# Performance work log

Hardware: AMD Instinct MI355X
Metric: run time of the kernel (lower is better)

The kernel has to match this reference:

```python
import jax, jax.numpy as jnp
import numpy as np

HEADS = 4
DIM_HEAD = 32


def setup_inputs() -> dict:
    key = jax.random.key(0)
    k1, k2, k3, k4 = jax.random.split(key, 4)
    dim = 256
    hidden = HEADS * DIM_HEAD  # 128
    x = jax.random.normal(k1, (4, dim, 64, 64), dtype=jnp.float32)
    # 1x1 convs are channel-mixing matmuls; store weights as [out_ch, in_ch]
    w_qkv = jax.random.normal(k2, (3 * hidden, dim), dtype=jnp.float32) * (dim ** -0.5)
    w_out = jax.random.normal(k3, (dim, hidden), dtype=jnp.float32) * (hidden ** -0.5)
    b_out = jax.random.normal(k4, (dim,), dtype=jnp.float32) * 0.02
    return {"x": x, "w_qkv": w_qkv, "w_out": w_out, "b_out": b_out}


def reference(x, w_qkv, w_out, b_out):
    b, c, h, w = x.shape
    n = h * w
    scale = DIM_HEAD ** -0.5
    xf = x.reshape(b, c, n)                                   # b c n
    qkv = jnp.einsum('oc,bcn->bon', w_qkv, xf)                # b (3*H*D) n
    q, k, v = jnp.split(qkv, 3, axis=1)                       # each b (H*D) n
    q = q.reshape(b, HEADS, DIM_HEAD, n) * scale              # b h d n
    k = k.reshape(b, HEADS, DIM_HEAD, n)
    v = v.reshape(b, HEADS, DIM_HEAD, n)
    sim = jnp.einsum('bhdi,bhdj->bhij', q, k)                 # b h n n
    attn = jax.nn.softmax(sim, axis=-1)                       # stable max-subtract inside
    out = jnp.einsum('bhij,bhdj->bhdi', attn, v)              # b h d n
    out = out.reshape(b, HEADS * DIM_HEAD, n)                 # b (h d) n
    out = jnp.einsum('oc,bcn->bon', w_out, out) + b_out[None, :, None]
    return out.reshape(b, -1, h, w)
```

## Files before the change

kernel.cpp:

```cpp
#include <hip/hip_runtime.h>
#include <hip/hip_bf16.h>
#include <stdint.h>

#define B_SZ 4
#define C_IN 256
#define N_SP 4096
#define HEADS 4
#define DH 32
#define HID 128

#define BI 128
#define BJ 64
#define JHALF 2048
#define PP 68

typedef short short4v __attribute__((ext_vector_type(4)));
typedef short short8 __attribute__((ext_vector_type(8)));
typedef float f32x4 __attribute__((ext_vector_type(4)));

#if __has_builtin(__builtin_amdgcn_exp2f)
#define EXP2 __builtin_amdgcn_exp2f
#else
#define EXP2 exp2f
#endif

__device__ __forceinline__ short f2bfs(float f) {
  return (short)((__float_as_uint(f) + 0x8000u) >> 16);
}
__device__ __forceinline__ float bfs2f(short s) {
  return __uint_as_float(((uint32_t)(unsigned short)s) << 16);
}
__device__ __forceinline__ short8 ld_frag(const short* p) {
  short4v a = *(const short4v*)p;
  short4v b = *(const short4v*)(p + 4);
  return __builtin_shufflevector(a, b, 0, 1, 2, 3, 4, 5, 6, 7);
}
__device__ __forceinline__ f32x4 mfma16(short8 a, short8 b, f32x4 c) {
  return __builtin_amdgcn_mfma_f32_16x16x32_bf16(a, b, c, 0, 0, 0);
}

__global__ __launch_bounds__(256) void prep_k(
    const float* __restrict__ x, const float* __restrict__ w_qkv,
    const float* __restrict__ w_out,
    short* __restrict__ xh, short* __restrict__ xl,
    short* __restrict__ wqh, short* __restrict__ wql,
    short* __restrict__ woh, short* __restrict__ wol) {
  const int t = threadIdx.x;
  const int bx = blockIdx.x;
  if (bx < 1024) {
    __shared__ float T[64 * 65];
    const int b = bx >> 8, n0 = ((bx >> 2) & 63) * 64, c0 = (bx & 3) * 64;
    const float* xb = x + (size_t)b * C_IN * N_SP;
    {
      const int n = t & 63, cw = t >> 6;
#pragma unroll
      for (int i = 0; i < 16; ++i) {
        const int c = cw * 16 + i;
        T[n * 65 + c] = xb[(size_t)(c0 + c) * N_SP + n0 + n];
      }
    }
    __syncthreads();
    {
      const int n = t >> 2, cg = t & 3;
#pragma unroll
      for (int j = 0; j < 2; ++j) {
        const int c = cg * 16 + j * 8;
        short8 hv, lv;
#pragma unroll
        for (int e = 0; e < 8; ++e) {
          const float v = T[n * 65 + c + e];
          const short hh = f2bfs(v);
          hv[e] = hh;
          lv[e] = f2bfs(v - bfs2f(hh));
        }
        const size_t off = ((size_t)(b * N_SP + n0 + n)) * C_IN + c0 + c;
        *(short8*)(xh + off) = hv;
        *(short8*)(xl + off) = lv;
      }
    }
  } else {
    const int f0 = (bx - 1024) * 8192;
#pragma unroll
    for (int j = 0; j < 32; ++j) {
      const int f = f0 + j * 256 + t;
      float v;
      short *dh, *dl;
      int idx;
      if (f < 384 * 256) { v = w_qkv[f]; dh = wqh; dl = wql; idx = f; }
      else { idx = f - 384 * 256; v = w_out[idx]; dh = woh; dl = wol; }
      const short hh = f2bfs(v);
      dh[idx] = hh;
      dl[idx] = f2bfs(v - bfs2f(hh));
    }
  }
}

__global__ __launch_bounds__(256) void qkv_mfma_k(
    const short* __restrict__ xh, const short* __restrict__ xl,
    const short* __restrict__ wqh, const short* __restrict__ wql,
    short* __restrict__ qt, short* __restrict__ kt, short* __restrict__ vt) {
  const int t = threadIdx.x;
  const int lane = t & 63, w = t >> 6;
  const int l15 = lane & 15, quad = lane >> 4;
  const int osec = blockIdx.y, b = blockIdx.z;
  const int n0 = blockIdx.x * 64 + w * 16;
  const size_t xrow = ((size_t)(b * N_SP + n0 + l15)) * C_IN;
  const size_t wrow = ((size_t)(osec * 128 + l15)) * C_IN;
  const bool isv = (osec == 2);
  const f32x4 zz = {0.f, 0.f, 0.f, 0.f};
  f32x4 acc[8];
#pragma unroll
  for (int ot = 0; ot < 8; ++ot) acc[ot] = zz;

  for (int k0 = 0; k0 < C_IN; k0 += 32) {
    const int ko = k0 + quad * 8;
    const short8 xhf = *(const short8*)(xh + xrow + ko);
    const short8 xlf = *(const short8*)(xl + xrow + ko);
#pragma unroll
    for (int ot = 0; ot < 8; ++ot) {
      const size_t wo = wrow + (size_t)ot * 16 * C_IN + ko;
      const short8 whf = *(const short8*)(wqh + wo);
      const short8 wlf = *(const short8*)(wql + wo);
      if (isv) {
        acc[ot] = mfma16(xhf, whf, acc[ot]);
        acc[ot] = mfma16(xlf, whf, acc[ot]);
        acc[ot] = mfma16(xhf, wlf, acc[ot]);
      } else {
        acc[ot] = mfma16(whf, xhf, acc[ot]);
        acc[ot] = mfma16(whf, xlf, acc[ot]);
        acc[ot] = mfma16(wlf, xhf, acc[ot]);
      }
    }
  }

  if (!isv) {
    const float sc = osec ? 1.f : (0.17677669529663687f * 1.4426950408889634f);
    short* dst = osec ? kt : qt;
    const int n = n0 + l15;
#pragma unroll
    for (int ot = 0; ot < 8; ++ot) {
      const int ol = ot * 16 + quad * 4;
      const int h = ol >> 5, d0 = ol & 31;
      short4v p;
#pragma unroll
      for (int r = 0; r < 4; ++r) p[r] = f2bfs(acc[ot][r] * sc);
      *(short4v*)(dst + ((size_t)(b * HEADS + h) * N_SP + n) * DH + d0) = p;
    }
  } else {
    const int n = n0 + quad * 4;
#pragma unroll
    for (int ot = 0; ot < 8; ++ot) {
      const int ol = ot * 16 + l15;
      const int h = ol >> 5, d = ol & 31;
      short4v p;
#pragma unroll
      for (int r = 0; r < 4; ++r) p[r] = f2bfs(acc[ot][r]);
      *(short4v*)(vt + ((size_t)(b * HEADS + h) * DH + d) * N_SP + n) = p;
    }
  }
}

__global__ __launch_bounds__(256, 2) void attn_k(
    const short* __restrict__ qt, const short* __restrict__ kt,
    const short* __restrict__ vt, float* __restrict__ po,
    float* __restrict__ lws) {
  __shared__ short Ps[BI * PP];
  const int t = threadIdx.x;
  const int lane = t & 63, w = t >> 6;
  const int l15 = lane & 15, quad = lane >> 4;
  const int i0 = blockIdx.x * BI;
  const int bh = blockIdx.y;
  const int part = blockIdx.z;
  const int jbase = part * JHALF;
  const short* qg = qt + ((size_t)bh * N_SP + i0) * DH;
  const short* kg = kt + ((size_t)bh * N_SP + jbase) * DH;
  const short* vg = vt + (size_t)bh * DH * N_SP + jbase;

  short8 bq[2];
#pragma unroll
  for (int tt = 0; tt < 2; ++tt)
    bq[tt] = *(const short8*)(qg + (size_t)(w * 32 + tt * 16 + l15) * DH + quad * 8);

  const f32x4 zz = {0.f, 0.f, 0.f, 0.f};
  f32x4 o_acc[2][2] = {{zz, zz}, {zz, zz}};
  f32x4 l_acc[2] = {zz, zz};
  short8 ones;
#pragma unroll
  for (int e = 0; e < 8; ++e) ones[e] = (short)0x3F80;
  short* prow[2];
#pragma unroll
  for (int tt = 0; tt < 2; ++tt) prow[tt] = Ps + (w * 32 + tt * 16 + l15) * PP;

  short8 akA[4], akB[4], vbA[2][2], vbB[2][2];
#pragma unroll
  for (int jt = 0; jt < 4; ++jt)
    akA[jt] = *(const short8*)(kg + (size_t)(jt * 16 + l15) * DH + quad * 8);
#pragma unroll
  for (int dt = 0; dt < 2; ++dt)
#pragma unroll
    for (int kk = 0; kk < 2; ++kk)
      vbA[dt][kk] = *(const short8*)(vg + (size_t)(dt * 16 + l15) * N_SP + kk * 32 + quad * 8);

  auto body = [&](const short8 (&akc)[4], const short8 (&vbc)[2][2],
                  short8 (&akn)[4], short8 (&vbn)[2][2], int jn) {
    f32x4 sf[2][4];
#pragma unroll
    for (int tt = 0; tt < 2; ++tt)
#pragma unroll
      for (int jt = 0; jt < 4; ++jt) sf[tt][jt] = mfma16(akc[jt], bq[tt], zz);
#pragma unroll
    for (int jt = 0; jt < 4; ++jt)
      akn[jt] = *(const short8*)(kg + (size_t)(jn + jt * 16 + l15) * DH + quad * 8);
#pragma unroll
    for (int dt = 0; dt < 2; ++dt)
#pragma unroll
      for (int kk = 0; kk < 2; ++kk)
        vbn[dt][kk] = *(const short8*)(vg + (size_t)(dt * 16 + l15) * N_SP + jn + kk * 32 + quad * 8);
#pragma unroll
    for (int tt = 0; tt < 2; ++tt)
#pragma unroll
      for (int jt = 0; jt < 4; ++jt) {
        const float e0 = EXP2(sf[tt][jt][0]);
        const float e1 = EXP2(sf[tt][jt][1]);
        const float e2 = EXP2(sf[tt][jt][2]);
        const float e3 = EXP2(sf[tt][jt][3]);
        uint2 pk;
        asm("v_cvt_pk_bf16_f32 %0, %1, %2" : "=v"(pk.x) : "v"(e0), "v"(e1));
        asm("v_cvt_pk_bf16_f32 %0, %1, %2" : "=v"(pk.y) : "v"(e2), "v"(e3));
        *(uint2*)(prow[tt] + jt * 16 + quad * 4) = pk;
      }
    asm volatile("s_waitcnt lgkmcnt(0)" ::: "memory");
    short8 pa[2][2];
#pragma unroll
    for (int tt = 0; tt < 2; ++tt)
#pragma unroll
      for (int kk = 0; kk < 2; ++kk) pa[tt][kk] = ld_frag(prow[tt] + kk * 32 + quad * 8);
#pragma unroll
    for (int tt = 0; tt < 2; ++tt) {
#pragma unroll
      for (int dt = 0; dt < 2; ++dt) {
        o_acc[tt][dt] = mfma16(pa[tt][0], vbc[dt][0], o_acc[tt][dt]);
        o_acc[tt][dt] = mfma16(pa[tt][1], vbc[dt][1], o_acc[tt][dt]);
      }
      l_acc[tt] = mfma16(pa[tt][0], ones, l_acc[tt]);
      l_acc[tt] = mfma16(pa[tt][1], ones, l_acc[tt]);
    }
  };

  for (int jo = 0; jo < JHALF; jo += 2 * BJ) {
    body(akA, vbA, akB, vbB, (jo + BJ) & (JHALF - 1));
    body(akB, vbB, akA, vbA, (jo + 2 * BJ) & (JHALF - 1));
  }

  if (l15 == 0) {
#pragma unroll
    for (int tt = 0; tt < 2; ++tt)
#pragma unroll
      for (int r = 0; r < 4; ++r)
        lws[((size_t)(part * 16 + bh)) * N_SP + i0 + w * 32 + tt * 16 + quad * 4 + r] =
            l_acc[tt][r];
  }
  {
    const int b = bh >> 2, h = bh & 3;
    float* pob = po + ((size_t)((part * B_SZ + b) * N_SP) + i0) * HID + h * 32;
#pragma unroll
    for (int tt = 0; tt < 2; ++tt)
#pragma unroll
      for (int dt = 0; dt < 2; ++dt)
#pragma unroll
        for (int r = 0; r < 4; ++r)
          pob[(size_t)(w * 32 + tt * 16 + quad * 4 + r) * HID + dt * 16 + l15] =
              o_acc[tt][dt][r];
  }
}

__global__ __launch_bounds__(256) void out_mfma_k(
    const float* __restrict__ po, const float* __restrict__ lws,
    const short* __restrict__ woh, const short* __restrict__ wol,
    const float* __restrict__ bias, float* __restrict__ out) {
  const int t = threadIdx.x;
  const int lane = t & 63, w = t >> 6;
  const int l15 = lane & 15, quad = lane >> 4;
  const int osec = blockIdx.y, b = blockIdx.z;
  const int n0 = blockIdx.x * 64 + w * 16;
  const int n = n0 + l15;
  const size_t PSTR = (size_t)B_SZ * N_SP * HID;
  const float* arow = po + ((size_t)(b * N_SP) + n) * HID;
  const size_t wrow = ((size_t)(osec * 128 + l15)) * HID;
  const f32x4 zz = {0.f, 0.f, 0.f, 0.f};
  f32x4 acc[8];
#pragma unroll
  for (int ot = 0; ot < 8; ++ot) acc[ot] = zz;

  for (int k0 = 0; k0 < HID; k0 += 32) {
    const int ko = k0 + quad * 8;
    const int h = k0 >> 5;
    const int bh = b * HEADS + h;
    const float lv = lws[(size_t)bh * N_SP + n] + lws[(size_t)(16 + bh) * N_SP + n];
    const float linv = 1.f / lv;
    const float* pr = arow + ko;
    const float4 u0 = *(const float4*)(pr);
    const float4 u1 = *(const float4*)(pr + 4);
    const float4 v0 = *(const float4*)(pr + PSTR);
    const float4 v1 = *(const float4*)(pr + PSTR + 4);
    const float av[8] = {(u0.x + v0.x) * linv, (u0.y + v0.y) * linv,
                         (u0.z + v0.z) * linv, (u0.w + v0.w) * linv,
                         (u1.x + v1.x) * linv, (u1.y + v1.y) * linv,
                         (u1.z + v1.z) * linv, (u1.w + v1.w) * linv};
    short8 ahf, alf;
#pragma unroll
    for (int e = 0; e < 8; ++e) {
      const short hh = f2bfs(av[e]);
      ahf[e] = hh;
      alf[e] = f2bfs(av[e] - bfs2f(hh));
    }
#pragma unroll
    for (int ot = 0; ot < 8; ++ot) {
      const size_t wo = wrow + (size_t)ot * 16 * HID + ko;
      const short8 whf = *(const short8*)(woh + wo);
      const short8 wlf = *(const short8*)(wol + wo);
      acc[ot] = mfma16(ahf, whf, acc[ot]);
      acc[ot] = mfma16(alf, whf, acc[ot]);
      acc[ot] = mfma16(ahf, wlf, acc[ot]);
    }
  }
#pragma unroll
  for (int ot = 0; ot < 8; ++ot) {
    const int o = osec * 128 + ot * 16 + l15;
    const float bv = bias[o];
    float4 v = make_float4(acc[ot][0] + bv, acc[ot][1] + bv,
                           acc[ot][2] + bv, acc[ot][3] + bv);
    *(float4*)(out + ((size_t)(b * C_IN + o)) * N_SP + n0 + quad * 4) = v;
  }
}

extern "C" void kernel_launch(void* const* d_in, const int* in_sizes, int n_in,
                              void* d_out, int out_size, void* d_ws, size_t ws_size,
                              hipStream_t stream) {
  const float* x = (const float*)d_in[0];
  const float* w_qkv = (const float*)d_in[1];
  const float* w_out = (const float*)d_in[2];
  const float* b_out = (const float*)d_in[3];
  float* out = (float*)d_out;

  short* xh = (short*)d_ws;
  short* xl = xh + (size_t)B_SZ * N_SP * C_IN;
  short* wqh = xl + (size_t)B_SZ * N_SP * C_IN;
  short* wql = wqh + 384 * C_IN;
  short* woh = wql + 384 * C_IN;
  short* wol = woh + C_IN * HID;
  short* qt = wol + C_IN * HID;
  short* kt = qt + (size_t)16 * N_SP * DH;
  short* vt = kt + (size_t)16 * N_SP * DH;
  float* lws = (float*)(vt + (size_t)16 * N_SP * DH);
  float* po = (float*)xh;

  prep_k<<<dim3(1040), 256, 0, stream>>>(x, w_qkv, w_out, xh, xl, wqh, wql, woh, wol);
  qkv_mfma_k<<<dim3(64, 3, B_SZ), 256, 0, stream>>>(xh, xl, wqh, wql, qt, kt, vt);
  attn_k<<<dim3(N_SP / BI, B_SZ * HEADS, 2), 256, 0, stream>>>(qt, kt, vt, po, lws);
  out_mfma_k<<<dim3(64, 2, B_SZ), 256, 0, stream>>>(po, lws, woh, wol, b_out, out);
}
```

Before: 248.7 us.

## Compute softmax row sums in VALU and cut registers for higher occupancy

Replaces the MFMA-with-ones row-sum accumulation with scalar float sums of the exponentials, reduced across quads with shuffles at the end. V fragments are no longer double-buffered across iterations; they are loaded at the start of each body, and S tiles are computed per row-tile so fewer live registers are needed. Launch bounds are raised from 2 to 4 blocks per CU to raise occupancy. The trade is less explicit prefetch of V and added VALU adds. The sums now use fp32 exponentials instead of bf16-rounded ones, which changes the normalisation slightly.

```diff
diff --git a/kernel.cpp b/kernel.cpp
--- a/kernel.cpp
+++ b/kernel.cpp
@@ -160,7 +160,7 @@
   }
 }
 
-__global__ __launch_bounds__(256, 2) void attn_k(
+__global__ __launch_bounds__(256, 4) void attn_k(
     const short* __restrict__ qt, const short* __restrict__ kt,
     const short* __restrict__ vt, float* __restrict__ po,
     float* __restrict__ lws) {
@@ -183,52 +183,44 @@
 
   const f32x4 zz = {0.f, 0.f, 0.f, 0.f};
   f32x4 o_acc[2][2] = {{zz, zz}, {zz, zz}};
-  f32x4 l_acc[2] = {zz, zz};
-  short8 ones;
-#pragma unroll
-  for (int e = 0; e < 8; ++e) ones[e] = (short)0x3F80;
+  float lsum[2] = {0.f, 0.f};
   short* prow[2];
 #pragma unroll
   for (int tt = 0; tt < 2; ++tt) prow[tt] = Ps + (w * 32 + tt * 16 + l15) * PP;
 
-  short8 akA[4], akB[4], vbA[2][2], vbB[2][2];
+  short8 akA[4], akB[4];
 #pragma unroll
   for (int jt = 0; jt < 4; ++jt)
     akA[jt] = *(const short8*)(kg + (size_t)(jt * 16 + l15) * DH + quad * 8);
-#pragma unroll
-  for (int dt = 0; dt < 2; ++dt)
-#pragma unroll
-    for (int kk = 0; kk < 2; ++kk)
-      vbA[dt][kk] = *(const short8*)(vg + (size_t)(dt * 16 + l15) * N_SP + kk * 32 + quad * 8);
-
-  auto body = [&](const short8 (&akc)[4], const short8 (&vbc)[2][2],
-                  short8 (&akn)[4], short8 (&vbn)[2][2], int jn) {
-    f32x4 sf[2][4];
-#pragma unroll
-    for (int tt = 0; tt < 2; ++tt)
-#pragma unroll
-      for (int jt = 0; jt < 4; ++jt) sf[tt][jt] = mfma16(akc[jt], bq[tt], zz);
+
+  auto body = [&](const short8 (&akc)[4], short8 (&akn)[4], int jcur, int jn) {
+    short8 vb[2][2];
+#pragma unroll
+    for (int dt = 0; dt < 2; ++dt)
+#pragma unroll
+      for (int kk = 0; kk < 2; ++kk)
+        vb[dt][kk] = *(const short8*)(vg + (size_t)(dt * 16 + l15) * N_SP + jcur + kk * 32 + quad * 8);
 #pragma unroll
     for (int jt = 0; jt < 4; ++jt)
       akn[jt] = *(const short8*)(kg + (size_t)(jn + jt * 16 + l15) * DH + quad * 8);
 #pragma unroll
-    for (int dt = 0; dt < 2; ++dt)
-#pragma unroll
-      for (int kk = 0; kk < 2; ++kk)
-        vbn[dt][kk] = *(const short8*)(vg + (size_t)(dt * 16 + l15) * N_SP + jn + kk * 32 + quad * 8);
-#pragma unroll
-    for (int tt = 0; tt < 2; ++tt)
+    for (int tt = 0; tt < 2; ++tt) {
+      f32x4 sf[4];
+#pragma unroll
+      for (int jt = 0; jt < 4; ++jt) sf[jt] = mfma16(akc[jt], bq[tt], zz);
 #pragma unroll
       for (int jt = 0; jt < 4; ++jt) {
-        const float e0 = EXP2(sf[tt][jt][0]);
-        const float e1 = EXP2(sf[tt][jt][1]);
-        const float e2 = EXP2(sf[tt][jt][2]);
-        const float e3 = EXP2(sf[tt][jt][3]);
+        const float e0 = EXP2(sf[jt][0]);
+        const float e1 = EXP2(sf[jt][1]);
+        const float e2 = EXP2(sf[jt][2]);
+        const float e3 = EXP2(sf[jt][3]);
+        lsum[tt] += (e0 + e1) + (e2 + e3);
         uint2 pk;
         asm("v_cvt_pk_bf16_f32 %0, %1, %2" : "=v"(pk.x) : "v"(e0), "v"(e1));
         asm("v_cvt_pk_bf16_f32 %0, %1, %2" : "=v"(pk.y) : "v"(e2), "v"(e3));
         *(uint2*)(prow[tt] + jt * 16 + quad * 4) = pk;
       }
+    }
     asm volatile("s_waitcnt lgkmcnt(0)" ::: "memory");
     short8 pa[2][2];
 #pragma unroll
@@ -236,29 +228,28 @@
 #pragma unroll
       for (int kk = 0; kk < 2; ++kk) pa[tt][kk] = ld_frag(prow[tt] + kk * 32 + quad * 8);
 #pragma unroll
-    for (int tt = 0; tt < 2; ++tt) {
+    for (int tt = 0; tt < 2; ++tt)
 #pragma unroll
       for (int dt = 0; dt < 2; ++dt) {
-        o_acc[tt][dt] = mfma16(pa[tt][0], vbc[dt][0], o_acc[tt][dt]);
-        o_acc[tt][dt] = mfma16(pa[tt][1], vbc[dt][1], o_acc[tt][dt]);
-      }
-      l_acc[tt] = mfma16(pa[tt][0], ones, l_acc[tt]);
-      l_acc[tt] = mfma16(pa[tt][1], ones, l_acc[tt]);
-    }
+        o_acc[tt][dt] = mfma16(pa[tt][0], vb[dt][0], o_acc[tt][dt]);
+        o_acc[tt][dt] = mfma16(pa[tt][1], vb[dt][1], o_acc[tt][dt]);
+      }
   };
 
   for (int jo = 0; jo < JHALF; jo += 2 * BJ) {
-    body(akA, vbA, akB, vbB, (jo + BJ) & (JHALF - 1));
-    body(akB, vbB, akA, vbA, (jo + 2 * BJ) & (JHALF - 1));
-  }
-
-  if (l15 == 0) {
+    body(akA, akB, jo, (jo + BJ) & (JHALF - 1));
+    body(akB, akA, jo + BJ, (jo + 2 * BJ) & (JHALF - 1));
+  }
+
+#pragma unroll
+  for (int tt = 0; tt < 2; ++tt) {
+    lsum[tt] += __shfl_xor(lsum[tt], 16);
+    lsum[tt] += __shfl_xor(lsum[tt], 32);
+  }
+  if (lane < 16) {
 #pragma unroll
     for (int tt = 0; tt < 2; ++tt)
-#pragma unroll
-      for (int r = 0; r < 4; ++r)
-        lws[((size_t)(part * 16 + bh)) * N_SP + i0 + w * 32 + tt * 16 + quad * 4 + r] =
-            l_acc[tt][r];
+      lws[((size_t)(part * 16 + bh)) * N_SP + i0 + w * 32 + tt * 16 + lane] = lsum[tt];
   }
   {
     const int b = bh >> 2, h = bh & 3;
```

New measurement: 248.9 us. About the same (+0.1%).
